# Kernel tuning notes

Hardware: AMD Instinct MI355X
Metric: run time of the kernel (lower is better)

The kernel has to match this reference:

```python
import jax, jax.numpy as jnp
import numpy as np

# ---- module constants (from init_kwargs) ----
VOXEL_SIZE = np.array([0.1, 0.1, 0.2], np.float32)
PC_RANGE = np.array([0.0, -40.0, -3.0, 70.4, 40.0, 1.0], np.float32)
MAX_PTS = 10            # max_points_in_voxel
MAX_VOX = 40000         # max_voxel_num (hard voxelization cap per sample)
GRID = np.round((PC_RANGE[3:] - PC_RANGE[:3]) / VOXEL_SIZE).astype(np.int32)  # [704,800,20] (x,y,z)
BIG = int(GRID[0]) * int(GRID[1]) * int(GRID[2])

PC_MIN = jnp.asarray(PC_RANGE[:3])
VSIZE = jnp.asarray(VOXEL_SIZE)
GRID_J = jnp.asarray(GRID)

B = 8
N_PER_B = 120000


def setup_inputs() -> dict:
    key = jax.random.key(0)
    k1, = jax.random.split(key, 1)
    u = jax.random.uniform(k1, (B * N_PER_B, 4), dtype=jnp.float32)
    # place points inside (and slightly around) pc_range
    x = u[:, 0] * 72.0 - 0.5
    y = u[:, 1] * 82.0 - 41.0
    z = u[:, 2] * 4.4 - 3.2
    inten = u[:, 3]
    bs_idx = jnp.repeat(jnp.arange(B, dtype=jnp.float32), N_PER_B)
    points = jnp.stack([bs_idx, x, y, z, inten], axis=1)  # [960000, 5]
    return {"points": points, "batch_size": B}


def _voxelize_one(pts):
    """Hard voxelization of one point cloud pts [N,4] -> fixed-size buffers.
    Faithful to first-come voxel ordering and per-voxel point caps."""
    N = pts.shape[0]
    idxs = jnp.arange(N, dtype=jnp.int32)
    xyz = pts[:, :3]
    c = jnp.floor((xyz - PC_MIN) / VSIZE).astype(jnp.int32)  # [N,3] (x,y,z)
    valid = jnp.all((c >= 0) & (c < GRID_J), axis=1)
    lid = (c[:, 2] * GRID[1] + c[:, 1]) * GRID[0] + c[:, 0]  # z-major linear id
    lid = jnp.where(valid, lid, BIG)

    order = jnp.argsort(lid)            # stable: within a voxel, original order kept
    lid_s = lid[order]
    is_new = jnp.concatenate([jnp.ones((1,), bool), lid_s[1:] != lid_s[:-1]])
    gid = jnp.cumsum(is_new.astype(jnp.int32)) - 1           # group id per sorted point
    starts = jax.lax.cummax(jnp.where(is_new, idxs, 0))      # group start position
    pos = idxs - starts                                      # rank inside its voxel

    g_lid = jax.ops.segment_min(lid_s, gid, num_segments=N)
    g_valid = g_lid < BIG
    first_orig = jax.ops.segment_min(order.astype(jnp.int32), gid, num_segments=N)
    # voxel slot = first-appearance rank (invalid/empty groups pushed to the end)
    first_key = jnp.where(g_valid, first_orig, N + idxs)
    perm = jnp.argsort(first_key)
    slot = jnp.zeros(N, jnp.int32).at[perm].set(idxs)

    pslot = slot[gid]
    keep = g_valid[gid] & (pslot < MAX_VOX) & (pos < MAX_PTS)
    sslot = jnp.where(keep, pslot, MAX_VOX)   # overflow bucket, sliced off
    spos = jnp.where(keep, pos, 0)
    voxels = jnp.zeros((MAX_VOX + 1, MAX_PTS, pts.shape[1]), pts.dtype)
    voxels = voxels.at[sslot, spos].set(pts[order])[:MAX_VOX]

    gcount = jax.ops.segment_sum(keep.astype(jnp.int32), gid, num_segments=N)
    gslot = jnp.where(g_valid & (slot < MAX_VOX), slot, MAX_VOX)
    num_points = jnp.zeros(MAX_VOX + 1, jnp.int32).at[gslot].set(gcount)[:MAX_VOX]

    cs = c[order]
    gz = jax.ops.segment_min(cs[:, 2], gid, num_segments=N)
    gy = jax.ops.segment_min(cs[:, 1], gid, num_segments=N)
    gx = jax.ops.segment_min(cs[:, 0], gid, num_segments=N)
    coors = jnp.full((MAX_VOX + 1, 3), -1, jnp.int32)
    coors = coors.at[gslot].set(jnp.stack([gz, gy, gx], axis=1))[:MAX_VOX]  # (z,y,x)
    return voxels, num_points, coors


def reference(points, batch_size):
    feats = points[:, 1:]
    n_per_b = feats.shape[0] // batch_size  # points constructed contiguously per sample
    pts = feats.reshape(batch_size, n_per_b, feats.shape[1])
    voxels_b, num_b, coors_b = jax.vmap(_voxelize_one)(pts)
    voxels = voxels_b.reshape(batch_size * MAX_VOX, MAX_PTS, feats.shape[1])
    num_points = num_b.reshape(-1)
    batch_col = jnp.repeat(jnp.arange(batch_size, dtype=jnp.int32), MAX_VOX)[:, None]
    coors_batch = jnp.concatenate([batch_col, coors_b.reshape(-1, 3)], axis=1)  # [b,z,y,x]
    grid_size = jnp.asarray(GRID)
    return voxels, num_points, coors_batch, grid_size
```

## Files before the change

### kernel.cpp

```cpp
#include <hip/hip_runtime.h>

#define NB        8
#define NPB       120000
#define NPTS      (NB * NPB)
#define MAX_PTS   10
#define MAX_VOX   40000
#define GX        704
#define GY        800
#define GZ        20

#define T0        (1 << 18)
#define T0MASK    (T0 - 1)

#define HC2       (1 << 15)
#define HMASK2    (HC2 - 1)
#define NSLOT2    (NB * HC2)

#define TILES     469
#define TILES_PAD 512
#define MBCAP     8192
#define MTILE     2048

#define EMPTY64   0xFFFFFFFFFFFFFFFFull

#define OUT_VOX   0LL
#define OUT_NUM   12800000LL
#define OUT_COOR  13120000LL
#define OUT_GRID  14400000LL

__device__ __forceinline__ bool point_cell(const float* __restrict__ p,
                                           int& cx, int& cy, int& cz) {
    cx = (int)floorf((p[1] - 0.0f)   / 0.1f);
    cy = (int)floorf((p[2] - (-40.0f)) / 0.1f);
    cz = (int)floorf((p[3] - (-3.0f))  / 0.2f);
    return (cx >= 0) & (cx < GX) & (cy >= 0) & (cy < GY) & (cz >= 0) & (cz < GZ);
}

__device__ __forceinline__ unsigned hashA(int lid) {
    return (((unsigned)lid * 2654435761u) >> 14) & T0MASK;
}
__device__ __forceinline__ unsigned hashB(int lid) {
    return (((unsigned)lid * 0x9E3779B1u) >> 13) & T0MASK;
}
__device__ __forceinline__ unsigned slab_hash(int lid) {
    return (((unsigned)lid * 2654435761u) >> 17) & HMASK2;
}

__device__ __forceinline__ void slab_insert(unsigned long long* __restrict__ base,
                                            int lid, int idx) {
    unsigned long long key = ((unsigned long long)(unsigned)lid << 32)
                           | (unsigned long long)(unsigned)idx;
    unsigned h = slab_hash(lid);
    while (true) {
        unsigned long long oo = atomicMin(base + h, key);
        if (oo == EMPTY64) break;
        if ((oo >> 32) == (key >> 32)) break;
        if (oo > key) key = oo;
        h = (h + 1) & HMASK2;
    }
}

__device__ __forceinline__ unsigned slab_find(const unsigned long long* __restrict__ base,
                                              int lid) {
    unsigned h = slab_hash(lid);
    while (true) {
        unsigned long long cur = base[h];
        if (cur == EMPTY64) return 0xFFFFFFFFu;
        if ((unsigned)(cur >> 32) == (unsigned)lid) return (unsigned)cur;
        h = (h + 1) & HMASK2;
    }
}

__global__ void k_init(const float* __restrict__ pts, float* __restrict__ out,
                       ulonglong2* __restrict__ slab2, unsigned* __restrict__ tblA,
                       unsigned* __restrict__ tblB, int* __restrict__ lid32,
                       unsigned* __restrict__ mcount) {
    int b = blockIdx.x & 7;
    int idx = (blockIdx.x >> 3) * 256 + threadIdx.x;
    if (idx < NPB) {
        int g = b * NPB + idx;
        const float* p = pts + (long long)g * 5;
        int cx, cy, cz;
        if (point_cell(p, cx, cy, cz)) {
            int lid = (cz * GY + cy) * GX + cx;
            lid32[g] = lid;
            tblA[b * T0 + hashA(lid)] = (unsigned)idx;
            tblB[b * T0 + hashB(lid)] = (unsigned)idx;
        } else {
            lid32[g] = -1;
        }
    }
    int t = blockIdx.x * 256 + threadIdx.x;
    if (t < NSLOT2 / 2) {
        ulonglong2 e2; e2.x = EMPTY64; e2.y = EMPTY64;
        slab2[t] = e2;
    }
    if (t < NB) mcount[t * 16] = 0u;
    if (t == 0) {
        out[OUT_GRID + 0] = 704.f;
        out[OUT_GRID + 1] = 800.f;
        out[OUT_GRID + 2] = 20.f;
    }
}

__global__ void k_l0(const int* __restrict__ lid32, const unsigned* __restrict__ tblA,
                     const unsigned* __restrict__ tblB, unsigned char* __restrict__ flag,
                     unsigned long long* __restrict__ slabB) {
    int b = blockIdx.x & 7;
    int idx = (blockIdx.x >> 3) * 256 + threadIdx.x;
    if (idx >= NPB) return;
    int g = b * NPB + idx;
    int lid = lid32[g];
    if (lid < 0) { flag[g] = 0; return; }
    unsigned w = tblA[b * T0 + hashA(lid)];
    if (lid32[b * NPB + (int)w] == lid) {
        if (w == (unsigned)idx) { flag[g] = 1; return; }
        flag[g] = 4;
        slab_insert(slabB + (size_t)b * HC2, lid, idx);
        return;
    }
    w = tblB[b * T0 + hashB(lid)];
    if (lid32[b * NPB + (int)w] == lid) {
        if (w == (unsigned)idx) { flag[g] = 1; return; }
        flag[g] = 4;
        slab_insert(slabB + (size_t)b * HC2, lid, idx);
        return;
    }
    flag[g] = 3;
    slab_insert(slabB + (size_t)b * HC2, lid, idx);
}

__global__ void k_p2c(const int* __restrict__ lid32, const unsigned* __restrict__ tblA,
                      const unsigned* __restrict__ tblB,
                      const unsigned long long* __restrict__ slabB,
                      unsigned char* __restrict__ flag, unsigned char* __restrict__ rank8,
                      int* __restrict__ tileSum, int2* __restrict__ mlist,
                      unsigned* __restrict__ mcount) {
    int b = blockIdx.x & 7;
    int tile = blockIdx.x >> 3;
    int t = threadIdx.x;
    int idx = tile * 256 + t;
    int g = b * NPB + idx;
    int f = 0;
    if (idx < NPB) {
        unsigned char pf = flag[g];
        if (pf) {
            int lid = lid32[g];
            const unsigned long long* base = slabB + (size_t)b * HC2;
            unsigned smin = slab_find(base, lid);
            unsigned leader;
            if (pf == 1) {
                leader = (smin < (unsigned)idx) ? smin : (unsigned)idx;
            } else if (pf == 4) {
                unsigned w = tblA[b * T0 + hashA(lid)];
                if (lid32[b * NPB + (int)w] != lid) w = tblB[b * T0 + hashB(lid)];
                leader = (smin < w) ? smin : w;
            } else {
                leader = smin;
            }
            if (leader == (unsigned)idx) {
                f = 1;
            } else {
                unsigned m = atomicAdd(&mcount[b * 16], 1u);
                if (m < MBCAP) mlist[(size_t)b * MBCAP + m] = make_int2((int)leader, idx);
            }
        }
    }
    __shared__ int sc[256];
    sc[t] = f;
    __syncthreads();
    for (int off = 1; off < 256; off <<= 1) {
        int x = sc[t];
        if (t >= off) x += sc[t - off];
        __syncthreads();
        sc[t] = x;
        __syncthreads();
    }
    if (idx < NPB) {
        flag[g] = (unsigned char)f;
        rank8[g] = (unsigned char)(sc[t] - f);
    }
    if (t == 255) tileSum[b * TILES_PAD + tile] = sc[255];
}

__global__ void k_finish(const float* __restrict__ pts, const int* __restrict__ lid32,
                         const unsigned char* __restrict__ flag,
                         const unsigned char* __restrict__ rank8,
                         const int* __restrict__ tileSum,
                         float* __restrict__ out, unsigned short* __restrict__ slotOf) {
    int b = blockIdx.x & 7;
    int tile = blockIdx.x >> 3;
    int t = threadIdx.x;

    __shared__ int sc[256];
    __shared__ int soff[TILES_PAD];
    int v0 = (2 * t     < TILES) ? tileSum[b * TILES_PAD + 2 * t]     : 0;
    int v1 = (2 * t + 1 < TILES) ? tileSum[b * TILES_PAD + 2 * t + 1] : 0;
    int w = v0 + v1;
    sc[t] = w;
    __syncthreads();
    for (int off = 1; off < 256; off <<= 1) {
        int x = sc[t];
        if (t >= off) x += sc[t - off];
        __syncthreads();
        sc[t] = x;
        __syncthreads();
    }
    int e = sc[t] - w;
    soff[2 * t] = e;
    soff[2 * t + 1] = e + v0;
    __syncthreads();

    int idx = tile * 256 + t;
    if (idx >= NPB) return;
    int g = b * NPB + idx;
    if (!flag[g]) return;

    int slot = soff[tile] + (int)rank8[g];
    slotOf[g] = (unsigned short)(slot < 65535 ? slot : 65535);
    if (slot >= MAX_VOX) return;
    int lid = lid32[g];
    unsigned ul = (unsigned)lid;
    unsigned cx = ul % (unsigned)GX;
    unsigned tt = ul / (unsigned)GX;
    unsigned cy = tt % (unsigned)GY;
    unsigned cz = tt / (unsigned)GY;
    long long r = (long long)b * MAX_VOX + slot;
    ((float4*)(out + OUT_COOR))[r] = make_float4((float)b, (float)cz, (float)cy, (float)cx);
    out[OUT_NUM + r] = 1.f;
    const float* p = pts + (long long)g * 5;
    float4* row = (float4*)(out + OUT_VOX) + (size_t)r * MAX_PTS;
    row[0] = make_float4(p[1], p[2], p[3], p[4]);
    float4 zf = make_float4(0.f, 0.f, 0.f, 0.f);
    #pragma unroll
    for (int i = 1; i < MAX_PTS; i++) row[i] = zf;
}

__global__ void k_multi(const float* __restrict__ pts,
                        const int2* __restrict__ mlist, const unsigned* __restrict__ mcount,
                        const unsigned short* __restrict__ slotOf,
                        float* __restrict__ out) {
    int b = blockIdx.y;
    unsigned n = mcount[b * 16];
    if (n > MBCAP) n = MBCAP;
    unsigned t = blockIdx.x * blockDim.x + threadIdx.x;
    const int2* lst = mlist + (size_t)b * MBCAP;
    bool active = (t < n);
    int2 e = active ? lst[t] : make_int2(-1, -1);
    int pos = 1;
    int same = 0;
    __shared__ int2 sm[MTILE];
    for (unsigned chunk = 0; chunk < n; chunk += MTILE) {
        unsigned m = n - chunk;
        if (m > MTILE) m = MTILE;
        for (unsigned i = threadIdx.x; i < m; i += 256)
            sm[i] = lst[chunk + i];
        __syncthreads();
        if (active) {
            #pragma unroll 4
            for (unsigned j = 0; j < m; j++) {
                int2 o = sm[j];
                if (o.x == e.x) { same++; if (o.y < e.y) pos++; }
            }
        }
        __syncthreads();
    }
    if (!active) return;
    int slot = (int)slotOf[(size_t)b * NPB + e.x];
    if (slot >= MAX_VOX) return;
    if (pos == 1) {
        int cnt = same + 1;
        out[OUT_NUM + (long long)b * MAX_VOX + slot] =
            (float)(cnt < MAX_PTS ? cnt : MAX_PTS);
    }
    if (pos >= MAX_PTS) return;
    const float* p = pts + ((long long)b * NPB + e.y) * 5;
    ((float4*)(out + OUT_VOX))[(long long)(b * MAX_VOX + slot) * MAX_PTS + pos] =
        make_float4(p[1], p[2], p[3], p[4]);
}

extern "C" void kernel_launch(void* const* d_in, const int* in_sizes, int n_in,
                              void* d_out, int out_size, void* d_ws, size_t ws_size,
                              hipStream_t stream) {
    const float* pts = (const float*)d_in[0];
    float* out = (float*)d_out;

    char* w = (char*)d_ws;
    unsigned* tblA = (unsigned*)w;            w += (size_t)NB * T0 * 4;
    unsigned* tblB = (unsigned*)w;            w += (size_t)NB * T0 * 4;
    unsigned long long* slabB = (unsigned long long*)w;
    w += (size_t)NSLOT2 * 8;
    int2* mlist = (int2*)w;  w += (size_t)NB * MBCAP * 8;
    int* lid32 = (int*)w;    w += (size_t)NPTS * 4;
    int* tileSum = (int*)w;  w += (size_t)NB * TILES_PAD * 4;
    unsigned* mcount = (unsigned*)w; w += (size_t)NB * 16 * 4;
    unsigned short* slotOf = (unsigned short*)w; w += (size_t)NPTS * 2;
    unsigned char* flag = (unsigned char*)w;  w += (size_t)NPTS;
    unsigned char* rank8 = (unsigned char*)w; w += (size_t)NPTS;

    const int PB = TILES * NB;
    k_init<<<dim3(PB), dim3(256), 0, stream>>>(pts, out, (ulonglong2*)slabB,
                                               tblA, tblB, lid32, mcount);
    k_l0<<<dim3(PB), dim3(256), 0, stream>>>(lid32, tblA, tblB, flag, slabB);
    k_p2c<<<dim3(PB), dim3(256), 0, stream>>>(lid32, tblA, tblB, slabB,
                                              flag, rank8, tileSum, mlist, mcount);
    k_finish<<<dim3(PB), dim3(256), 0, stream>>>(pts, lid32, flag, rank8, tileSum,
                                                 out, slotOf);
    k_multi<<<dim3(MBCAP / 256, NB), dim3(256), 0, stream>>>(pts, mlist, mcount, slotOf, out);
}
```

Measured before the change: 161.1 us.

## Store lid in claim tables and replace per-point leader search with slab sweep

The claim tables now hold 64-bit (lid, idx) keys, so a claim can be verified without an indirect lid32 lookup. Leader resolution for non-claimers moves to a sweep over occupied slab slots, which fixes flags for each voxel's minimum index. A wave-level count kernel then enumerates only non-leader points into the multi-point list, and the per-tile rank scan moves into k_finish, which removes the rank8 buffer. This adds a kernel launch and doubles the claim-table footprint, and it relies on every inserted lid being present in the slab when slab_find drops its empty-slot check.

```diff
diff --git a/kernel.cpp b/kernel.cpp
--- a/kernel.cpp
+++ b/kernel.cpp
@@ -65,16 +65,26 @@
     unsigned h = slab_hash(lid);
     while (true) {
         unsigned long long cur = base[h];
-        if (cur == EMPTY64) return 0xFFFFFFFFu;
         if ((unsigned)(cur >> 32) == (unsigned)lid) return (unsigned)cur;
         h = (h + 1) & HMASK2;
     }
 }
 
+__device__ __forceinline__ unsigned claimer_of(const unsigned long long* __restrict__ tA,
+                                               const unsigned long long* __restrict__ tB,
+                                               int b, int lid) {
+    unsigned long long v = tA[(size_t)b * T0 + hashA(lid)];
+    if ((unsigned)(v >> 32) == (unsigned)lid) return (unsigned)v;
+    v = tB[(size_t)b * T0 + hashB(lid)];
+    if ((unsigned)(v >> 32) == (unsigned)lid) return (unsigned)v;
+    return 0xFFFFFFFFu;
+}
+
 __global__ void k_init(const float* __restrict__ pts, float* __restrict__ out,
-                       ulonglong2* __restrict__ slab2, unsigned* __restrict__ tblA,
-                       unsigned* __restrict__ tblB, int* __restrict__ lid32,
-                       unsigned* __restrict__ mcount) {
+                       ulonglong2* __restrict__ slab2,
+                       unsigned long long* __restrict__ tblA,
+                       unsigned long long* __restrict__ tblB,
+                       int* __restrict__ lid32, unsigned* __restrict__ mcount) {
     int b = blockIdx.x & 7;
     int idx = (blockIdx.x >> 3) * 256 + threadIdx.x;
     if (idx < NPB) {
@@ -84,8 +94,10 @@
         if (point_cell(p, cx, cy, cz)) {
             int lid = (cz * GY + cy) * GX + cx;
             lid32[g] = lid;
-            tblA[b * T0 + hashA(lid)] = (unsigned)idx;
-            tblB[b * T0 + hashB(lid)] = (unsigned)idx;
+            unsigned long long key = ((unsigned long long)(unsigned)lid << 32)
+                                   | (unsigned long long)(unsigned)idx;
+            tblA[(size_t)b * T0 + hashA(lid)] = key;
+            tblB[(size_t)b * T0 + hashB(lid)] = key;
         } else {
             lid32[g] = -1;
         }
@@ -103,8 +115,10 @@
     }
 }
 
-__global__ void k_l0(const int* __restrict__ lid32, const unsigned* __restrict__ tblA,
-                     const unsigned* __restrict__ tblB, unsigned char* __restrict__ flag,
+__global__ void k_l0(const int* __restrict__ lid32,
+                     const unsigned long long* __restrict__ tblA,
+                     const unsigned long long* __restrict__ tblB,
+                     unsigned char* __restrict__ flag,
                      unsigned long long* __restrict__ slabB) {
     int b = blockIdx.x & 7;
     int idx = (blockIdx.x >> 3) * 256 + threadIdx.x;
@@ -112,80 +126,80 @@
     int g = b * NPB + idx;
     int lid = lid32[g];
     if (lid < 0) { flag[g] = 0; return; }
-    unsigned w = tblA[b * T0 + hashA(lid)];
-    if (lid32[b * NPB + (int)w] == lid) {
-        if (w == (unsigned)idx) { flag[g] = 1; return; }
-        flag[g] = 4;
+    unsigned long long v = tblA[(size_t)b * T0 + hashA(lid)];
+    if ((unsigned)(v >> 32) == (unsigned)lid) {
+        if ((unsigned)v == (unsigned)idx) { flag[g] = 1; return; }
+        flag[g] = 0;
         slab_insert(slabB + (size_t)b * HC2, lid, idx);
         return;
     }
-    w = tblB[b * T0 + hashB(lid)];
-    if (lid32[b * NPB + (int)w] == lid) {
-        if (w == (unsigned)idx) { flag[g] = 1; return; }
-        flag[g] = 4;
+    v = tblB[(size_t)b * T0 + hashB(lid)];
+    if ((unsigned)(v >> 32) == (unsigned)lid) {
+        if ((unsigned)v == (unsigned)idx) { flag[g] = 1; return; }
+        flag[g] = 0;
         slab_insert(slabB + (size_t)b * HC2, lid, idx);
         return;
     }
-    flag[g] = 3;
+    flag[g] = 0;
     slab_insert(slabB + (size_t)b * HC2, lid, idx);
 }
 
-__global__ void k_p2c(const int* __restrict__ lid32, const unsigned* __restrict__ tblA,
-                      const unsigned* __restrict__ tblB,
-                      const unsigned long long* __restrict__ slabB,
-                      unsigned char* __restrict__ flag, unsigned char* __restrict__ rank8,
-                      int* __restrict__ tileSum, int2* __restrict__ mlist,
-                      unsigned* __restrict__ mcount) {
-    int b = blockIdx.x & 7;
-    int tile = blockIdx.x >> 3;
-    int t = threadIdx.x;
-    int idx = tile * 256 + t;
-    int g = b * NPB + idx;
-    int f = 0;
-    if (idx < NPB) {
-        unsigned char pf = flag[g];
-        if (pf) {
-            int lid = lid32[g];
-            const unsigned long long* base = slabB + (size_t)b * HC2;
-            unsigned smin = slab_find(base, lid);
-            unsigned leader;
-            if (pf == 1) {
-                leader = (smin < (unsigned)idx) ? smin : (unsigned)idx;
-            } else if (pf == 4) {
-                unsigned w = tblA[b * T0 + hashA(lid)];
-                if (lid32[b * NPB + (int)w] != lid) w = tblB[b * T0 + hashB(lid)];
-                leader = (smin < w) ? smin : w;
-            } else {
-                leader = smin;
-            }
-            if (leader == (unsigned)idx) {
-                f = 1;
-            } else {
+__global__ void k_sweep(const unsigned long long* __restrict__ slabB,
+                        const unsigned long long* __restrict__ tblA,
+                        const unsigned long long* __restrict__ tblB,
+                        unsigned char* __restrict__ flag) {
+    int s = blockIdx.x * 256 + threadIdx.x;
+    unsigned long long v = slabB[s];
+    if (v == EMPTY64) return;
+    int b = s >> 15;
+    int lid = (int)(unsigned)(v >> 32);
+    unsigned smin = (unsigned)v;
+    unsigned cl = claimer_of(tblA, tblB, b, lid);
+    if (cl == 0xFFFFFFFFu) {
+        flag[b * NPB + (int)smin] = 1;
+    } else if (smin < cl) {
+        flag[b * NPB + (int)cl] = 0;
+        flag[b * NPB + (int)smin] = 1;
+    }
+}
+
+__global__ void k_count(const unsigned* __restrict__ flag32, const int* __restrict__ lid32,
+                        const unsigned long long* __restrict__ slabB,
+                        const unsigned long long* __restrict__ tblA,
+                        const unsigned long long* __restrict__ tblB,
+                        int* __restrict__ tileSum, int2* __restrict__ mlist,
+                        unsigned* __restrict__ mcount) {
+    int w = blockIdx.x * 4 + ((int)threadIdx.x >> 6);
+    int lane = threadIdx.x & 63;
+    int b = w & 7;
+    int tile = w >> 3;
+    int i = tile * 64 + lane;
+    unsigned x = 0u;
+    if (i < NPB / 4) {
+        x = flag32[b * (NPB / 4) + i];
+        int4 l4 = ((const int4*)lid32)[b * (NPB / 4) + i];
+        #pragma unroll
+        for (int k = 0; k < 4; k++) {
+            int lk = (k == 0) ? l4.x : (k == 1) ? l4.y : (k == 2) ? l4.z : l4.w;
+            if (((x >> (8 * k)) & 255u) == 0u && lk >= 0) {
+                unsigned smin = slab_find(slabB + (size_t)b * HC2, lk);
+                unsigned cl = claimer_of(tblA, tblB, b, lk);
+                unsigned leader = (smin < cl) ? smin : cl;
+                int idx = i * 4 + k;
                 unsigned m = atomicAdd(&mcount[b * 16], 1u);
-                if (m < MBCAP) mlist[(size_t)b * MBCAP + m] = make_int2((int)leader, idx);
+                if (m < MBCAP)
+                    mlist[(size_t)b * MBCAP + m] = make_int2((int)leader, idx);
             }
         }
     }
-    __shared__ int sc[256];
-    sc[t] = f;
-    __syncthreads();
-    for (int off = 1; off < 256; off <<= 1) {
-        int x = sc[t];
-        if (t >= off) x += sc[t - off];
-        __syncthreads();
-        sc[t] = x;
-        __syncthreads();
-    }
-    if (idx < NPB) {
-        flag[g] = (unsigned char)f;
-        rank8[g] = (unsigned char)(sc[t] - f);
-    }
-    if (t == 255) tileSum[b * TILES_PAD + tile] = sc[255];
+    int s = (int)((x * 0x01010101u) >> 24);
+    #pragma unroll
+    for (int off = 32; off; off >>= 1) s += __shfl_down(s, off);
+    if (lane == 0) tileSum[b * TILES_PAD + tile] = s;
 }
 
 __global__ void k_finish(const float* __restrict__ pts, const int* __restrict__ lid32,
                          const unsigned char* __restrict__ flag,
-                         const unsigned char* __restrict__ rank8,
                          const int* __restrict__ tileSum,
                          float* __restrict__ out, unsigned short* __restrict__ slotOf) {
     int b = blockIdx.x & 7;
@@ -212,11 +226,22 @@
     __syncthreads();
 
     int idx = tile * 256 + t;
-    if (idx >= NPB) return;
     int g = b * NPB + idx;
-    if (!flag[g]) return;
-
-    int slot = soff[tile] + (int)rank8[g];
+    int f = (idx < NPB) ? (int)flag[g] : 0;
+    sc[t] = f;
+    __syncthreads();
+    for (int off = 1; off < 256; off <<= 1) {
+        int x = sc[t];
+        if (t >= off) x += sc[t - off];
+        __syncthreads();
+        sc[t] = x;
+        __syncthreads();
+    }
+    int rank = sc[t] - f;
+
+    if (idx >= NPB || !f) return;
+
+    int slot = soff[tile] + rank;
     slotOf[g] = (unsigned short)(slot < 65535 ? slot : 65535);
     if (slot >= MAX_VOX) return;
     int lid = lid32[g];
@@ -286,8 +311,8 @@
     float* out = (float*)d_out;
 
     char* w = (char*)d_ws;
-    unsigned* tblA = (unsigned*)w;            w += (size_t)NB * T0 * 4;
-    unsigned* tblB = (unsigned*)w;            w += (size_t)NB * T0 * 4;
+    unsigned long long* tblA = (unsigned long long*)w; w += (size_t)NB * T0 * 8;
+    unsigned long long* tblB = (unsigned long long*)w; w += (size_t)NB * T0 * 8;
     unsigned long long* slabB = (unsigned long long*)w;
     w += (size_t)NSLOT2 * 8;
     int2* mlist = (int2*)w;  w += (size_t)NB * MBCAP * 8;
@@ -296,15 +321,15 @@
     unsigned* mcount = (unsigned*)w; w += (size_t)NB * 16 * 4;
     unsigned short* slotOf = (unsigned short*)w; w += (size_t)NPTS * 2;
     unsigned char* flag = (unsigned char*)w;  w += (size_t)NPTS;
-    unsigned char* rank8 = (unsigned char*)w; w += (size_t)NPTS;
 
     const int PB = TILES * NB;
     k_init<<<dim3(PB), dim3(256), 0, stream>>>(pts, out, (ulonglong2*)slabB,
                                                tblA, tblB, lid32, mcount);
     k_l0<<<dim3(PB), dim3(256), 0, stream>>>(lid32, tblA, tblB, flag, slabB);
-    k_p2c<<<dim3(PB), dim3(256), 0, stream>>>(lid32, tblA, tblB, slabB,
-                                              flag, rank8, tileSum, mlist, mcount);
-    k_finish<<<dim3(PB), dim3(256), 0, stream>>>(pts, lid32, flag, rank8, tileSum,
-                                                 out, slotOf);
+    k_sweep<<<dim3(NSLOT2 / 256), dim3(256), 0, stream>>>(slabB, tblA, tblB, flag);
+    k_count<<<dim3(TILES * NB / 4), dim3(256), 0, stream>>>((const unsigned*)flag, lid32,
+                                                            slabB, tblA, tblB,
+                                                            tileSum, mlist, mcount);
+    k_finish<<<dim3(PB), dim3(256), 0, stream>>>(pts, lid32, flag, tileSum, out, slotOf);
     k_multi<<<dim3(MBCAP / 256, NB), dim3(256), 0, stream>>>(pts, mlist, mcount, slotOf, out);
 }
```

Result: slower. 167.0 us (+3.6%).
